# Kernel tuning notes

Measured on AMD Instinct MI355X. Metric: run time of the kernel, lower is better.

## Reference

```python
import jax, jax.numpy as jnp
import numpy as np

N = 100_000   # number of sparse points
C = 128       # channels
K3 = 27       # 3x3x3 kernel offsets


def sparse_conv(x, nbr, W, b):
    """Minkowski-style sparse conv: gather-GEMM-scatter.
    x:   [N, Cin] point features
    nbr: [N, K3] neighbor index per kernel offset; index N -> missing (zero row)
    W:   [K3, Cin, Cout], b: [Cout]
    """
    x_pad = jnp.concatenate([x, jnp.zeros((1, x.shape[1]), x.dtype)], axis=0)

    def step(acc, wk_nk):
        Wk, nk = wk_nk                      # Wk: [Cin,Cout], nk: [N]
        return acc + x_pad[nk] @ Wk, None   # gather + GEMM, accumulate

    acc0 = jnp.broadcast_to(b, (x.shape[0], W.shape[2])).astype(x.dtype)
    acc, _ = jax.lax.scan(step, acc0, (W, nbr.T))
    return acc


def setup_inputs() -> dict:
    key = jax.random.key(0)
    ks = jax.random.split(key, 12)
    Ch = C // 2

    def w(k, shape, fan_in):
        return jax.random.normal(k, shape, dtype=jnp.float32) / np.sqrt(fan_in)

    x = jax.random.normal(ks[0], (N, C), dtype=jnp.float32)
    # neighbor map; value N means "no neighbor" (maps to zero-padded row)
    nbr = jax.random.randint(ks[1], (N, K3), 0, N + 1, dtype=jnp.int32)

    return {
        "x": x,
        "nbr": nbr,
        "W00": w(ks[2], (K3, C, Ch), K3 * C),   # conv0_0: kxkxk, C -> C/2
        "b00": jnp.zeros((Ch,), jnp.float32),
        "W01": w(ks[3], (K3, Ch, Ch), K3 * Ch),  # conv0_1: kxkxk, C/2 -> C/2
        "b01": jnp.zeros((Ch,), jnp.float32),
        "W10": w(ks[4], (C, Ch), C),             # conv1_0: 1x1x1, C -> C/2
        "b10": jnp.zeros((Ch,), jnp.float32),
        "W11": w(ks[5], (K3, Ch, Ch), K3 * Ch),  # conv1_1: kxkxk, C/2 -> C/2
        "b11": jnp.zeros((Ch,), jnp.float32),
        "W12": w(ks[6], (Ch, Ch), Ch),           # conv1_2: 1x1x1, C/2 -> C/2
        "b12": jnp.zeros((Ch,), jnp.float32),
    }


def reference(x, nbr, W00, b00, W01, b01, W10, b10, W11, b11, W12, b12):
    # branch 0: conv -> relu -> conv
    h0 = jax.nn.relu(sparse_conv(x, nbr, W00, b00))
    out0 = sparse_conv(h0, nbr, W01, b01)
    # branch 1: 1x1 conv -> relu -> conv -> relu -> 1x1 conv
    h1 = jax.nn.relu(x @ W10 + b10)
    h1 = jax.nn.relu(sparse_conv(h1, nbr, W11, b11))
    out1 = h1 @ W12 + b12
    # concat channels, residual add
    return jnp.concatenate([out0, out1], axis=1) + x
```

## Files before the change

### kernel.cpp

```cpp
#include <hip/hip_runtime.h>
#include <hip/hip_bf16.h>
#include <stdint.h>

typedef __bf16 bf16x8 __attribute__((ext_vector_type(8)));
typedef float  f32x4  __attribute__((ext_vector_type(4)));

#define MFMA(A, B, C) __builtin_amdgcn_mfma_f32_16x16x32_bf16((A), (B), (C), 0, 0, 0)

#define LDS_BARRIER() asm volatile("s_waitcnt lgkmcnt(0)\n\ts_barrier" ::: "memory")

static __device__ __forceinline__ unsigned short f2b(float f) {
    union { float f; unsigned int u; } v; v.f = f;
    return (unsigned short)((v.u + 0x7FFFu + ((v.u >> 16) & 1u)) >> 16);
}

__global__ __launch_bounds__(256) void convert_kernel(
    const float* __restrict__ x, unsigned short* __restrict__ xb,
    unsigned short* __restrict__ hb, int N) {
    long long i = (long long)blockIdx.x * blockDim.x + threadIdx.x;
    long long base = i * 4;
    long long nx = (long long)N * 128;
    long long total = nx + 128;
    if (base >= total) return;
    if (base < nx) {
        float4 v = *(const float4*)(x + base);
        ushort4 o;
        o.x = f2b(v.x); o.y = f2b(v.y); o.z = f2b(v.z); o.w = f2b(v.w);
        *(ushort4*)(xb + base) = o;
    } else {
        ushort4 z = make_ushort4(0, 0, 0, 0);
        *(ushort4*)(xb + base) = z;
        *(ushort4*)(hb + base) = z;
    }
}

__global__ __launch_bounds__(256) void pack_kernel(
    const float* __restrict__ W00, const float* __restrict__ W01,
    const float* __restrict__ W10, const float* __restrict__ W11,
    const float* __restrict__ W12,
    unsigned short* __restrict__ wp00, unsigned short* __restrict__ wpC,
    unsigned short* __restrict__ wp10, unsigned short* __restrict__ wp12) {
    int g = blockIdx.x * blockDim.x + threadIdx.x;
    const float* W; int cinSteps; int which;
    if (g < 27648)      { W = W00; cinSteps = 4; which = 0; }
    else if (g < 41472) { g -= 27648; W = W01; cinSteps = 2; which = 1; }
    else if (g < 55296) { g -= 41472; W = W11; cinSteps = 2; which = 2; }
    else if (g < 56320) { g -= 55296; W = W10; cinSteps = 4; which = 3; }
    else if (g < 56832) { g -= 56320; W = W12; cinSteps = 2; which = 4; }
    else return;
    int lane = g & 63;
    int st   = g >> 6;
    int t    = st & 3;
    int s    = st >> 2;
    int q = lane >> 4, n16 = lane & 15;
    int k    = s / cinSteps;
    int cinb = (s % cinSteps) * 32;
    int Cin  = cinSteps * 32;
    int cout = t * 16 + n16;
    unsigned short o[8];
#pragma unroll
    for (int j = 0; j < 8; ++j) {
        float v = W[(size_t)(k * Cin + cinb + q * 8 + j) * 64 + cout];
        o[j] = f2b(v);
    }
    unsigned short* dst;
    if (which == 0)      dst = wp00 + (size_t)g * 8;
    else if (which == 1) dst = wpC + (size_t)k * 8192 +
                               ((size_t)(((s & 1) * 4 + t) * 64 + lane)) * 8;
    else if (which == 2) dst = wpC + (size_t)k * 8192 + 4096 +
                               ((size_t)(((s & 1) * 4 + t) * 64 + lane)) * 8;
    else if (which == 3) dst = wp10 + (size_t)g * 8;
    else                 dst = wp12 + (size_t)g * 8;
    *(ushort4*)(dst)     = make_ushort4(o[0], o[1], o[2], o[3]);
    *(ushort4*)(dst + 4) = make_ushort4(o[4], o[5], o[6], o[7]);
}

__global__ __launch_bounds__(256, 3) void passB_kernel(
    const unsigned short* __restrict__ xb, const int* __restrict__ nbr,
    const unsigned short* __restrict__ wp00, const unsigned short* __restrict__ wp10,
    const float* __restrict__ b00, const float* __restrict__ b10,
    unsigned short* __restrict__ hb, int N) {
    __shared__ __align__(16) unsigned short bbuf[2][8192];
    __shared__ int lds_idx[128 * 27];
    const int tid  = threadIdx.x;
    const int lane = tid & 63;
    const int wv   = tid >> 6;
    const int q = lane >> 4, n16 = lane & 15;
    const int rowbase = blockIdx.x * 128 + wv * 32;

    int4 br[4];
#pragma unroll
    for (int j = 0; j < 4; ++j) br[j] = *(const int4*)(wp00 + j * 2048 + tid * 8);
    {
        long long gbase = (long long)blockIdx.x * 128 * 27;
        long long lim = (long long)N * 27 - 1;
        for (int i = tid; i < 3456; i += 256) {
            long long gi = gbase + i; if (gi > lim) gi = lim;
            lds_idx[i] = nbr[gi];
        }
    }
#pragma unroll
    for (int j = 0; j < 4; ++j) *(int4*)(&bbuf[0][j * 2048 + tid * 8]) = br[j];
    __syncthreads();

    f32x4 acc0[2][4];
    f32x4 acc1[2][4];
#pragma unroll
    for (int rs = 0; rs < 2; ++rs)
#pragma unroll
        for (int t = 0; t < 4; ++t) { acc0[rs][t] = (f32x4)0.f; acc1[rs][t] = (f32x4)0.f; }

    const int idxb0 = (wv * 32 + n16) * 27;
    const int idxb1 = (wv * 32 + 16 + n16) * 27;
    const int own0 = min(rowbase + n16, N - 1);
    const int own1 = min(rowbase + 16 + n16, N - 1);

    int ia = lds_idx[idxb0], ib = lds_idx[idxb1];
    bf16x8 D0[4], D1[4];
    {
        const unsigned short* p0 = xb + (size_t)ia * 128 + q * 8;
        const unsigned short* p1 = xb + (size_t)ib * 128 + q * 8;
#pragma unroll
        for (int s2 = 0; s2 < 4; ++s2) {
            D0[s2] = *(const bf16x8*)(p0 + s2 * 32);
            D1[s2] = *(const bf16x8*)(p1 + s2 * 32);
        }
    }

    for (int k = 0; k < 27; ++k) {
        int buf = k & 1;
        if (k < 26) {
            const unsigned short* src = wp00 + (size_t)(k + 1) * 8192;
#pragma unroll
            for (int j = 0; j < 4; ++j) br[j] = *(const int4*)(src + j * 2048 + tid * 8);
        }
        int ian = (k + 1 < 27) ? lds_idx[idxb0 + k + 1] : own0;
        int ibn = (k + 1 < 27) ? lds_idx[idxb1 + k + 1] : own1;
        bf16x8 D0n[4], D1n[4];
        {
            const unsigned short* p0 = xb + (size_t)ian * 128 + q * 8;
            const unsigned short* p1 = xb + (size_t)ibn * 128 + q * 8;
#pragma unroll
            for (int s2 = 0; s2 < 4; ++s2) {
                D0n[s2] = *(const bf16x8*)(p0 + s2 * 32);
                D1n[s2] = *(const bf16x8*)(p1 + s2 * 32);
            }
        }
        const unsigned short* lb = &bbuf[buf][0];
#pragma unroll
        for (int s2 = 0; s2 < 4; ++s2) {
#pragma unroll
            for (int t = 0; t < 4; ++t) {
                bf16x8 B = *(const bf16x8*)(lb + (s2 * 4 + t) * 512 + lane * 8);
                acc0[0][t] = MFMA(D0[s2], B, acc0[0][t]);
                acc0[1][t] = MFMA(D1[s2], B, acc0[1][t]);
            }
        }
        if (k < 26) {
#pragma unroll
            for (int j = 0; j < 4; ++j)
                *(int4*)(&bbuf[buf ^ 1][j * 2048 + tid * 8]) = br[j];
        }
#pragma unroll
        for (int s2 = 0; s2 < 4; ++s2) { D0[s2] = D0n[s2]; D1[s2] = D1n[s2]; }
        LDS_BARRIER();
    }

#pragma unroll
    for (int s2 = 0; s2 < 4; ++s2) {
#pragma unroll
        for (int t = 0; t < 4; ++t) {
            bf16x8 B = *(const bf16x8*)(wp10 + s2 * 2048 + t * 512 + lane * 8);
            acc1[0][t] = MFMA(D0[s2], B, acc1[0][t]);
            acc1[1][t] = MFMA(D1[s2], B, acc1[1][t]);
        }
    }

#pragma unroll
    for (int rs = 0; rs < 2; ++rs)
#pragma unroll
        for (int t = 0; t < 4; ++t) {
            int col = t * 16 + n16;
            float bb0 = b00[col], bb1 = b10[col];
#pragma unroll
            for (int r = 0; r < 4; ++r) {
                int row = rowbase + rs * 16 + q * 4 + r;
                if (row < N) {
                    hb[(size_t)row * 128 + col]      = f2b(fmaxf(acc0[rs][t][r] + bb0, 0.f));
                    hb[(size_t)row * 128 + 64 + col] = f2b(fmaxf(acc1[rs][t][r] + bb1, 0.f));
                }
            }
        }
}

__global__ __launch_bounds__(256, 3) void passC_kernel(
    const unsigned short* __restrict__ hb, const int* __restrict__ nbr,
    const float* __restrict__ x,
    const unsigned short* __restrict__ wpC, const unsigned short* __restrict__ wp12,
    const float* __restrict__ b01, const float* __restrict__ b11,
    const float* __restrict__ b12, float* __restrict__ out, int N) {
    __shared__ __align__(16) unsigned short bbuf[2][8192];
    __shared__ int lds_idx[128 * 27];
    const int tid  = threadIdx.x;
    const int lane = tid & 63;
    const int wv   = tid >> 6;
    const int q = lane >> 4, n16 = lane & 15;
    const int rowbase = blockIdx.x * 128 + wv * 32;

    int4 br[4];
#pragma unroll
    for (int j = 0; j < 4; ++j) br[j] = *(const int4*)(wpC + j * 2048 + tid * 8);
    {
        long long gbase = (long long)blockIdx.x * 128 * 27;
        long long lim = (long long)N * 27 - 1;
        for (int i = tid; i < 3456; i += 256) {
            long long gi = gbase + i; if (gi > lim) gi = lim;
            lds_idx[i] = nbr[gi];
        }
    }
#pragma unroll
    for (int j = 0; j < 4; ++j) *(int4*)(&bbuf[0][j * 2048 + tid * 8]) = br[j];
    __syncthreads();

    f32x4 accO0[2][4];
    f32x4 accT[2][4];
#pragma unroll
    for (int rs = 0; rs < 2; ++rs)
#pragma unroll
        for (int t = 0; t < 4; ++t) { accO0[rs][t] = (f32x4)0.f; accT[rs][t] = (f32x4)0.f; }

    const int idxb0 = (wv * 32 + n16) * 27;
    const int idxb1 = (wv * 32 + 16 + n16) * 27;

    int ia = lds_idx[idxb0], ib = lds_idx[idxb1];
    bf16x8 DA0[2], DC0[2], DA1[2], DC1[2];
    {
        const unsigned short* p0 = hb + (size_t)ia * 128 + q * 8;
        const unsigned short* p1 = hb + (size_t)ib * 128 + q * 8;
#pragma unroll
        for (int s2 = 0; s2 < 2; ++s2) {
            DA0[s2] = *(const bf16x8*)(p0 + s2 * 32);
            DC0[s2] = *(const bf16x8*)(p0 + 64 + s2 * 32);
            DA1[s2] = *(const bf16x8*)(p1 + s2 * 32);
            DC1[s2] = *(const bf16x8*)(p1 + 64 + s2 * 32);
        }
    }

    for (int k = 0; k < 27; ++k) {
        int buf = k & 1;
        if (k < 26) {
            const unsigned short* src = wpC + (size_t)(k + 1) * 8192;
#pragma unroll
            for (int j = 0; j < 4; ++j) br[j] = *(const int4*)(src + j * 2048 + tid * 8);
        }
        bf16x8 DA0n[2], DC0n[2], DA1n[2], DC1n[2];
        if (k < 26) {
            int ian = lds_idx[idxb0 + k + 1];
            int ibn = lds_idx[idxb1 + k + 1];
            const unsigned short* p0 = hb + (size_t)ian * 128 + q * 8;
            const unsigned short* p1 = hb + (size_t)ibn * 128 + q * 8;
#pragma unroll
            for (int s2 = 0; s2 < 2; ++s2) {
                DA0n[s2] = *(const bf16x8*)(p0 + s2 * 32);
                DC0n[s2] = *(const bf16x8*)(p0 + 64 + s2 * 32);
                DA1n[s2] = *(const bf16x8*)(p1 + s2 * 32);
                DC1n[s2] = *(const bf16x8*)(p1 + 64 + s2 * 32);
            }
        }
        const unsigned short* lb = &bbuf[buf][0];
#pragma unroll
        for (int s2 = 0; s2 < 2; ++s2) {
#pragma unroll
            for (int t = 0; t < 4; ++t) {
                bf16x8 B = *(const bf16x8*)(lb + (s2 * 4 + t) * 512 + lane * 8);
                accO0[0][t] = MFMA(DA0[s2], B, accO0[0][t]);
                accO0[1][t] = MFMA(DA1[s2], B, accO0[1][t]);
            }
#pragma unroll
            for (int t = 0; t < 4; ++t) {
                bf16x8 B2 = *(const bf16x8*)(lb + 4096 + (s2 * 4 + t) * 512 + lane * 8);
                accT[0][t] = MFMA(DC0[s2], B2, accT[0][t]);
                accT[1][t] = MFMA(DC1[s2], B2, accT[1][t]);
            }
        }
        if (k < 26) {
#pragma unroll
            for (int j = 0; j < 4; ++j)
                *(int4*)(&bbuf[buf ^ 1][j * 2048 + tid * 8]) = br[j];
#pragma unroll
            for (int s2 = 0; s2 < 2; ++s2) {
                DA0[s2] = DA0n[s2]; DC0[s2] = DC0n[s2];
                DA1[s2] = DA1n[s2]; DC1[s2] = DC1n[s2];
            }
        }
        LDS_BARRIER();
    }

    unsigned short* scratch = &bbuf[0][0];
    unsigned short* myl = scratch + wv * 2304;
#pragma unroll
    for (int rs = 0; rs < 2; ++rs)
#pragma unroll
        for (int t = 0; t < 4; ++t) {
            int col = t * 16 + n16;
            float bo = b01[col], bt = b11[col];
#pragma unroll
            for (int r = 0; r < 4; ++r) {
                int row = rowbase + rs * 16 + q * 4 + r;
                if (row < N) {
                    float xv = __builtin_nontemporal_load(x + (size_t)row * 128 + col);
                    __builtin_nontemporal_store(accO0[rs][t][r] + bo + xv,
                                                out + (size_t)row * 128 + col);
                }
                float tv = fmaxf(accT[rs][t][r] + bt, 0.f);
                myl[(rs * 16 + q * 4 + r) * 72 + col] = f2b(tv);
            }
        }

    f32x4 accO1[2][4];
#pragma unroll
    for (int rs = 0; rs < 2; ++rs)
#pragma unroll
        for (int t = 0; t < 4; ++t) accO1[rs][t] = (f32x4)0.f;
#pragma unroll
    for (int s2 = 0; s2 < 2; ++s2) {
        bf16x8 A0 = *(const bf16x8*)(myl + n16 * 72 + s2 * 32 + q * 8);
        bf16x8 A1 = *(const bf16x8*)(myl + (16 + n16) * 72 + s2 * 32 + q * 8);
#pragma unroll
        for (int t = 0; t < 4; ++t) {
            bf16x8 B = *(const bf16x8*)(wp12 + s2 * 2048 + t * 512 + lane * 8);
            accO1[0][t] = MFMA(A0, B, accO1[0][t]);
            accO1[1][t] = MFMA(A1, B, accO1[1][t]);
        }
    }
#pragma unroll
    for (int rs = 0; rs < 2; ++rs)
#pragma unroll
        for (int t = 0; t < 4; ++t) {
            int col = t * 16 + n16;
            float bo = b12[col];
#pragma unroll
            for (int r = 0; r < 4; ++r) {
                int row = rowbase + rs * 16 + q * 4 + r;
                if (row < N) {
                    float xv = __builtin_nontemporal_load(x + (size_t)row * 128 + 64 + col);
                    __builtin_nontemporal_store(accO1[rs][t][r] + bo + xv,
                                                out + (size_t)row * 128 + 64 + col);
                }
            }
        }
}

extern "C" void kernel_launch(void* const* d_in, const int* in_sizes, int n_in,
                              void* d_out, int out_size, void* d_ws, size_t ws_size,
                              hipStream_t stream) {
    const float* x   = (const float*)d_in[0];
    const int*   nbr = (const int*)d_in[1];
    const float* W00 = (const float*)d_in[2];
    const float* b00 = (const float*)d_in[3];
    const float* W01 = (const float*)d_in[4];
    const float* b01 = (const float*)d_in[5];
    const float* W10 = (const float*)d_in[6];
    const float* b10 = (const float*)d_in[7];
    const float* W11 = (const float*)d_in[8];
    const float* b11 = (const float*)d_in[9];
    const float* W12 = (const float*)d_in[10];
    const float* b12 = (const float*)d_in[11];
    float* out = (float*)d_out;
    int N = in_sizes[0] / 128;

    char* ws = (char*)d_ws;
    size_t cur = 0;
    unsigned short* xb  = (unsigned short*)(ws + cur); cur += (size_t)(N + 1) * 128 * 2;
    unsigned short* hb  = (unsigned short*)(ws + cur); cur += (size_t)(N + 1) * 128 * 2;
    unsigned short* wp00 = (unsigned short*)(ws + cur); cur += 27648 * 8 * 2;
    unsigned short* wpC  = (unsigned short*)(ws + cur); cur += (size_t)27 * 8192 * 2;
    unsigned short* wp10 = (unsigned short*)(ws + cur); cur += 8192 * 2;
    unsigned short* wp12 = (unsigned short*)(ws + cur); cur += 4096 * 2;

    long long cvt_groups = ((long long)N * 128 + 128) / 4;
    int cvt_blocks = (int)((cvt_groups + 255) / 256);
    convert_kernel<<<cvt_blocks, 256, 0, stream>>>(x, xb, hb, N);
    pack_kernel<<<222, 256, 0, stream>>>(W00, W01, W10, W11, W12,
                                         wp00, wpC, wp10, wp12);
    int nstrips = (N + 127) / 128;
    passB_kernel<<<nstrips, 256, 0, stream>>>(xb, nbr, wp00, wp10, b00, b10, hb, N);
    passC_kernel<<<nstrips, 256, 0, stream>>>(hb, nbr, x, wpC, wp12,
                                              b01, b11, b12, out, N);
}
```

Before: 430.1 us.

## Double rows per wave to reuse each LDS weight fragment across four row tiles

Each wave now handles 64 rows (four 16-row tiles) instead of 32, so each block covers 256 points and every B fragment read from LDS feeds four MFMAs instead of two. This halves the number of blocks and the total weight streaming and barrier count per point. In exchange it doubles accumulator and gather registers, so occupancy drops from three to two blocks per SIMD-group. It also needs a larger index buffer in LDS, which is reused as scratch for the fourth wave's epilogue.

```diff
diff --git a/kernel.cpp b/kernel.cpp
--- a/kernel.cpp
+++ b/kernel.cpp
@@ -75,26 +75,26 @@
     *(ushort4*)(dst + 4) = make_ushort4(o[4], o[5], o[6], o[7]);
 }
 
-__global__ __launch_bounds__(256, 3) void passB_kernel(
+__global__ __launch_bounds__(256, 2) void passB_kernel(
     const unsigned short* __restrict__ xb, const int* __restrict__ nbr,
     const unsigned short* __restrict__ wp00, const unsigned short* __restrict__ wp10,
     const float* __restrict__ b00, const float* __restrict__ b10,
     unsigned short* __restrict__ hb, int N) {
     __shared__ __align__(16) unsigned short bbuf[2][8192];
-    __shared__ int lds_idx[128 * 27];
+    __shared__ __align__(16) int lds_idx[256 * 27];
     const int tid  = threadIdx.x;
     const int lane = tid & 63;
     const int wv   = tid >> 6;
     const int q = lane >> 4, n16 = lane & 15;
-    const int rowbase = blockIdx.x * 128 + wv * 32;
+    const int rowbase = blockIdx.x * 256 + wv * 64;
 
     int4 br[4];
 #pragma unroll
     for (int j = 0; j < 4; ++j) br[j] = *(const int4*)(wp00 + j * 2048 + tid * 8);
     {
-        long long gbase = (long long)blockIdx.x * 128 * 27;
+        long long gbase = (long long)blockIdx.x * 256 * 27;
         long long lim = (long long)N * 27 - 1;
-        for (int i = tid; i < 3456; i += 256) {
+        for (int i = tid; i < 6912; i += 256) {
             long long gi = gbase + i; if (gi > lim) gi = lim;
             lds_idx[i] = nbr[gi];
         }
@@ -103,28 +103,26 @@
     for (int j = 0; j < 4; ++j) *(int4*)(&bbuf[0][j * 2048 + tid * 8]) = br[j];
     __syncthreads();
 
-    f32x4 acc0[2][4];
-    f32x4 acc1[2][4];
-#pragma unroll
-    for (int rs = 0; rs < 2; ++rs)
+    f32x4 acc0[4][4];
+    f32x4 acc1[4][4];
+#pragma unroll
+    for (int rs = 0; rs < 4; ++rs)
 #pragma unroll
         for (int t = 0; t < 4; ++t) { acc0[rs][t] = (f32x4)0.f; acc1[rs][t] = (f32x4)0.f; }
 
-    const int idxb0 = (wv * 32 + n16) * 27;
-    const int idxb1 = (wv * 32 + 16 + n16) * 27;
-    const int own0 = min(rowbase + n16, N - 1);
-    const int own1 = min(rowbase + 16 + n16, N - 1);
-
-    int ia = lds_idx[idxb0], ib = lds_idx[idxb1];
-    bf16x8 D0[4], D1[4];
-    {
-        const unsigned short* p0 = xb + (size_t)ia * 128 + q * 8;
-        const unsigned short* p1 = xb + (size_t)ib * 128 + q * 8;
-#pragma unroll
-        for (int s2 = 0; s2 < 4; ++s2) {
-            D0[s2] = *(const bf16x8*)(p0 + s2 * 32);
-            D1[s2] = *(const bf16x8*)(p1 + s2 * 32);
-        }
+    int idxb[4], own[4];
+#pragma unroll
+    for (int rs = 0; rs < 4; ++rs) {
+        idxb[rs] = (wv * 64 + rs * 16 + n16) * 27;
+        own[rs]  = min(rowbase + rs * 16 + n16, N - 1);
+    }
+
+    bf16x8 D[4][4];
+#pragma unroll
+    for (int rs = 0; rs < 4; ++rs) {
+        const unsigned short* p = xb + (size_t)lds_idx[idxb[rs]] * 128 + q * 8;
+#pragma unroll
+        for (int s2 = 0; s2 < 4; ++s2) D[rs][s2] = *(const bf16x8*)(p + s2 * 32);
     }
 
     for (int k = 0; k < 27; ++k) {
@@ -134,17 +132,13 @@
 #pragma unroll
             for (int j = 0; j < 4; ++j) br[j] = *(const int4*)(src + j * 2048 + tid * 8);
         }
-        int ian = (k + 1 < 27) ? lds_idx[idxb0 + k + 1] : own0;
-        int ibn = (k + 1 < 27) ? lds_idx[idxb1 + k + 1] : own1;
-        bf16x8 D0n[4], D1n[4];
-        {
-            const unsigned short* p0 = xb + (size_t)ian * 128 + q * 8;
-            const unsigned short* p1 = xb + (size_t)ibn * 128 + q * 8;
-#pragma unroll
-            for (int s2 = 0; s2 < 4; ++s2) {
-                D0n[s2] = *(const bf16x8*)(p0 + s2 * 32);
-                D1n[s2] = *(const bf16x8*)(p1 + s2 * 32);
-            }
+        bf16x8 Dn[4][4];
+#pragma unroll
+        for (int rs = 0; rs < 4; ++rs) {
+            int ian = (k + 1 < 27) ? lds_idx[idxb[rs] + k + 1] : own[rs];
+            const unsigned short* p = xb + (size_t)ian * 128 + q * 8;
+#pragma unroll
+            for (int s2 = 0; s2 < 4; ++s2) Dn[rs][s2] = *(const bf16x8*)(p + s2 * 32);
         }
         const unsigned short* lb = &bbuf[buf][0];
 #pragma unroll
@@ -152,8 +146,9 @@
 #pragma unroll
             for (int t = 0; t < 4; ++t) {
                 bf16x8 B = *(const bf16x8*)(lb + (s2 * 4 + t) * 512 + lane * 8);
-                acc0[0][t] = MFMA(D0[s2], B, acc0[0][t]);
-                acc0[1][t] = MFMA(D1[s2], B, acc0[1][t]);
+#pragma unroll
+                for (int rs = 0; rs < 4; ++rs)
+                    acc0[rs][t] = MFMA(D[rs][s2], B, acc0[rs][t]);
             }
         }
         if (k < 26) {
@@ -162,7 +157,9 @@
                 *(int4*)(&bbuf[buf ^ 1][j * 2048 + tid * 8]) = br[j];
         }
 #pragma unroll
-        for (int s2 = 0; s2 < 4; ++s2) { D0[s2] = D0n[s2]; D1[s2] = D1n[s2]; }
+        for (int rs = 0; rs < 4; ++rs)
+#pragma unroll
+            for (int s2 = 0; s2 < 4; ++s2) D[rs][s2] = Dn[rs][s2];
         LDS_BARRIER();
     }
 
@@ -171,13 +168,14 @@
 #pragma unroll
         for (int t = 0; t < 4; ++t) {
             bf16x8 B = *(const bf16x8*)(wp10 + s2 * 2048 + t * 512 + lane * 8);
-            acc1[0][t] = MFMA(D0[s2], B, acc1[0][t]);
-            acc1[1][t] = MFMA(D1[s2], B, acc1[1][t]);
-        }
-    }
-
-#pragma unroll
-    for (int rs = 0; rs < 2; ++rs)
+#pragma unroll
+            for (int rs = 0; rs < 4; ++rs)
+                acc1[rs][t] = MFMA(D[rs][s2], B, acc1[rs][t]);
+        }
+    }
+
+#pragma unroll
+    for (int rs = 0; rs < 4; ++rs)
 #pragma unroll
         for (int t = 0; t < 4; ++t) {
             int col = t * 16 + n16;
@@ -193,27 +191,27 @@
         }
 }
 
-__global__ __launch_bounds__(256, 3) void passC_kernel(
+__global__ __launch_bounds__(256, 2) void passC_kernel(
     const unsigned short* __restrict__ hb, const int* __restrict__ nbr,
     const float* __restrict__ x,
     const unsigned short* __restrict__ wpC, const unsigned short* __restrict__ wp12,
     const float* __restrict__ b01, const float* __restrict__ b11,
     const float* __restrict__ b12, float* __restrict__ out, int N) {
     __shared__ __align__(16) unsigned short bbuf[2][8192];
-    __shared__ int lds_idx[128 * 27];
+    __shared__ __align__(16) int lds_idx[256 * 27];
     const int tid  = threadIdx.x;
     const int lane = tid & 63;
     const int wv   = tid >> 6;
     const int q = lane >> 4, n16 = lane & 15;
-    const int rowbase = blockIdx.x * 128 + wv * 32;
+    const int rowbase = blockIdx.x * 256 + wv * 64;
 
     int4 br[4];
 #pragma unroll
     for (int j = 0; j < 4; ++j) br[j] = *(const int4*)(wpC + j * 2048 + tid * 8);
     {
-        long long gbase = (long long)blockIdx.x * 128 * 27;
+        long long gbase = (long long)blockIdx.x * 256 * 27;
         long long lim = (long long)N * 27 - 1;
-        for (int i = tid; i < 3456; i += 256) {
+        for (int i = tid; i < 6912; i += 256) {
             long long gi = gbase + i; if (gi > lim) gi = lim;
             lds_idx[i] = nbr[gi];
         }
@@ -222,27 +220,25 @@
     for (int j = 0; j < 4; ++j) *(int4*)(&bbuf[0][j * 2048 + tid * 8]) = br[j];
     __syncthreads();
 
-    f32x4 accO0[2][4];
-    f32x4 accT[2][4];
-#pragma unroll
-    for (int rs = 0; rs < 2; ++rs)
+    f32x4 accO0[4][4];
+    f32x4 accT[4][4];
+#pragma unroll
+    for (int rs = 0; rs < 4; ++rs)
 #pragma unroll
         for (int t = 0; t < 4; ++t) { accO0[rs][t] = (f32x4)0.f; accT[rs][t] = (f32x4)0.f; }
 
-    const int idxb0 = (wv * 32 + n16) * 27;
-    const int idxb1 = (wv * 32 + 16 + n16) * 27;
-
-    int ia = lds_idx[idxb0], ib = lds_idx[idxb1];
-    bf16x8 DA0[2], DC0[2], DA1[2], DC1[2];
-    {
-        const unsigned short* p0 = hb + (size_t)ia * 128 + q * 8;
-        const unsigned short* p1 = hb + (size_t)ib * 128 + q * 8;
+    int idxb[4];
+#pragma unroll
+    for (int rs = 0; rs < 4; ++rs) idxb[rs] = (wv * 64 + rs * 16 + n16) * 27;
+
+    bf16x8 DA[4][2], DC[4][2];
+#pragma unroll
+    for (int rs = 0; rs < 4; ++rs) {
+        const unsigned short* p = hb + (size_t)lds_idx[idxb[rs]] * 128 + q * 8;
 #pragma unroll
         for (int s2 = 0; s2 < 2; ++s2) {
-            DA0[s2] = *(const bf16x8*)(p0 + s2 * 32);
-            DC0[s2] = *(const bf16x8*)(p0 + 64 + s2 * 32);
-            DA1[s2] = *(const bf16x8*)(p1 + s2 * 32);
-            DC1[s2] = *(const bf16x8*)(p1 + 64 + s2 * 32);
+            DA[rs][s2] = *(const bf16x8*)(p + s2 * 32);
+            DC[rs][s2] = *(const bf16x8*)(p + 64 + s2 * 32);
         }
     }
 
@@ -253,18 +249,17 @@
 #pragma unroll
             for (int j = 0; j < 4; ++j) br[j] = *(const int4*)(src + j * 2048 + tid * 8);
         }
-        bf16x8 DA0n[2], DC0n[2], DA1n[2], DC1n[2];
-        if (k < 26) {
-            int ian = lds_idx[idxb0 + k + 1];
-            int ibn = lds_idx[idxb1 + k + 1];
-            const unsigned short* p0 = hb + (size_t)ian * 128 + q * 8;
-            const unsigned short* p1 = hb + (size_t)ibn * 128 + q * 8;
-#pragma unroll
-            for (int s2 = 0; s2 < 2; ++s2) {
-                DA0n[s2] = *(const bf16x8*)(p0 + s2 * 32);
-                DC0n[s2] = *(const bf16x8*)(p0 + 64 + s2 * 32);
-                DA1n[s2] = *(const bf16x8*)(p1 + s2 * 32);
-                DC1n[s2] = *(const bf16x8*)(p1 + 64 + s2 * 32);
+        bf16x8 DAn[4][2], DCn[4][2];
+        if (k < 26) {
+#pragma unroll
+            for (int rs = 0; rs < 4; ++rs) {
+                int ian = lds_idx[idxb[rs] + k + 1];
+                const unsigned short* p = hb + (size_t)ian * 128 + q * 8;
+#pragma unroll
+                for (int s2 = 0; s2 < 2; ++s2) {
+                    DAn[rs][s2] = *(const bf16x8*)(p + s2 * 32);
+                    DCn[rs][s2] = *(const bf16x8*)(p + 64 + s2 * 32);
+                }
             }
         }
         const unsigned short* lb = &bbuf[buf][0];
@@ -273,14 +268,16 @@
 #pragma unroll
             for (int t = 0; t < 4; ++t) {
                 bf16x8 B = *(const bf16x8*)(lb + (s2 * 4 + t) * 512 + lane * 8);
-                accO0[0][t] = MFMA(DA0[s2], B, accO0[0][t]);
-                accO0[1][t] = MFMA(DA1[s2], B, accO0[1][t]);
+#pragma unroll
+                for (int rs = 0; rs < 4; ++rs)
+                    accO0[rs][t] = MFMA(DA[rs][s2], B, accO0[rs][t]);
             }
 #pragma unroll
             for (int t = 0; t < 4; ++t) {
                 bf16x8 B2 = *(const bf16x8*)(lb + 4096 + (s2 * 4 + t) * 512 + lane * 8);
-                accT[0][t] = MFMA(DC0[s2], B2, accT[0][t]);
-                accT[1][t] = MFMA(DC1[s2], B2, accT[1][t]);
+#pragma unroll
+                for (int rs = 0; rs < 4; ++rs)
+                    accT[rs][t] = MFMA(DC[rs][s2], B2, accT[rs][t]);
             }
         }
         if (k < 26) {
@@ -288,18 +285,19 @@
             for (int j = 0; j < 4; ++j)
                 *(int4*)(&bbuf[buf ^ 1][j * 2048 + tid * 8]) = br[j];
 #pragma unroll
-            for (int s2 = 0; s2 < 2; ++s2) {
-                DA0[s2] = DA0n[s2]; DC0[s2] = DC0n[s2];
-                DA1[s2] = DA1n[s2]; DC1[s2] = DC1n[s2];
-            }
+            for (int rs = 0; rs < 4; ++rs)
+#pragma unroll
+                for (int s2 = 0; s2 < 2; ++s2) {
+                    DA[rs][s2] = DAn[rs][s2]; DC[rs][s2] = DCn[rs][s2];
+                }
         }
         LDS_BARRIER();
     }
 
-    unsigned short* scratch = &bbuf[0][0];
-    unsigned short* myl = scratch + wv * 2304;
-#pragma unroll
-    for (int rs = 0; rs < 2; ++rs)
+    unsigned short* myl = (wv < 3) ? (&bbuf[0][0] + wv * 4608)
+                                   : (unsigned short*)lds_idx;
+#pragma unroll
+    for (int rs = 0; rs < 4; ++rs)
 #pragma unroll
         for (int t = 0; t < 4; ++t) {
             int col = t * 16 + n16;
@@ -317,24 +315,25 @@
             }
         }
 
-    f32x4 accO1[2][4];
-#pragma unroll
-    for (int rs = 0; rs < 2; ++rs)
+    f32x4 accO1[4][4];
+#pragma unroll
+    for (int rs = 0; rs < 4; ++rs)
 #pragma unroll
         for (int t = 0; t < 4; ++t) accO1[rs][t] = (f32x4)0.f;
 #pragma unroll
     for (int s2 = 0; s2 < 2; ++s2) {
-        bf16x8 A0 = *(const bf16x8*)(myl + n16 * 72 + s2 * 32 + q * 8);
-        bf16x8 A1 = *(const bf16x8*)(myl + (16 + n16) * 72 + s2 * 32 + q * 8);
 #pragma unroll
         for (int t = 0; t < 4; ++t) {
             bf16x8 B = *(const bf16x8*)(wp12 + s2 * 2048 + t * 512 + lane * 8);
-            accO1[0][t] = MFMA(A0, B, accO1[0][t]);
-            accO1[1][t] = MFMA(A1, B, accO1[1][t]);
-        }
-    }
-#pragma unroll
-    for (int rs = 0; rs < 2; ++rs)
+#pragma unroll
+            for (int rs = 0; rs < 4; ++rs) {
+                bf16x8 A = *(const bf16x8*)(myl + (rs * 16 + n16) * 72 + s2 * 32 + q * 8);
+                accO1[rs][t] = MFMA(A, B, accO1[rs][t]);
+            }
+        }
+    }
+#pragma unroll
+    for (int rs = 0; rs < 4; ++rs)
 #pragma unroll
         for (int t = 0; t < 4; ++t) {
             int col = t * 16 + n16;
@@ -383,7 +382,7 @@
     convert_kernel<<<cvt_blocks, 256, 0, stream>>>(x, xb, hb, N);
     pack_kernel<<<222, 256, 0, stream>>>(W00, W01, W10, W11, W12,
                                          wp00, wpC, wp10, wp12);
-    int nstrips = (N + 127) / 128;
+    int nstrips = (N + 255) / 256;
     passB_kernel<<<nstrips, 256, 0, stream>>>(xb, nbr, wp00, wp10, b00, b10, hb, N);
     passC_kernel<<<nstrips, 256, 0, stream>>>(hb, nbr, x, wpC, wp12,
                                               b01, b11, b12, out, N);
```

Result: faster. 416.0 us (-3.3%).

## Split sparse-conv passes into channel-half phases with two-deep gather prefetch

Applied to the files above, without the earlier changes.

Both conv kernels now walk the input channels (passB) or the two output branches (passC) in two sequential phases of 64 channels. Each phase keeps a smaller weight double-buffer in LDS and holds only half-width gathered rows in registers. The freed registers and LDS pay for a prefetch two offsets ahead instead of one, to hide gather latency better. The cost is a second pass over the neighbour indices and repeated weight streaming, and each gathered row is now read in two halves, so gather traffic is less coalesced.

```diff
diff --git a/kernel.cpp b/kernel.cpp
--- a/kernel.cpp
+++ b/kernel.cpp
@@ -80,29 +80,14 @@
     const unsigned short* __restrict__ wp00, const unsigned short* __restrict__ wp10,
     const float* __restrict__ b00, const float* __restrict__ b10,
     unsigned short* __restrict__ hb, int N) {
-    __shared__ __align__(16) unsigned short bbuf[2][8192];
-    __shared__ int lds_idx[128 * 27];
+    __shared__ __align__(16) unsigned short bbuf[2][4096];
+    __shared__ __align__(16) int lds_idx[128 * 27];
     const int tid  = threadIdx.x;
     const int lane = tid & 63;
     const int wv   = tid >> 6;
     const int q = lane >> 4, n16 = lane & 15;
     const int rowbase = blockIdx.x * 128 + wv * 32;
 
-    int4 br[4];
-#pragma unroll
-    for (int j = 0; j < 4; ++j) br[j] = *(const int4*)(wp00 + j * 2048 + tid * 8);
-    {
-        long long gbase = (long long)blockIdx.x * 128 * 27;
-        long long lim = (long long)N * 27 - 1;
-        for (int i = tid; i < 3456; i += 256) {
-            long long gi = gbase + i; if (gi > lim) gi = lim;
-            lds_idx[i] = nbr[gi];
-        }
-    }
-#pragma unroll
-    for (int j = 0; j < 4; ++j) *(int4*)(&bbuf[0][j * 2048 + tid * 8]) = br[j];
-    __syncthreads();
-
     f32x4 acc0[2][4];
     f32x4 acc1[2][4];
 #pragma unroll
@@ -110,69 +95,95 @@
 #pragma unroll
         for (int t = 0; t < 4; ++t) { acc0[rs][t] = (f32x4)0.f; acc1[rs][t] = (f32x4)0.f; }
 
-    const int idxb0 = (wv * 32 + n16) * 27;
-    const int idxb1 = (wv * 32 + 16 + n16) * 27;
-    const int own0 = min(rowbase + n16, N - 1);
-    const int own1 = min(rowbase + 16 + n16, N - 1);
-
-    int ia = lds_idx[idxb0], ib = lds_idx[idxb1];
-    bf16x8 D0[4], D1[4];
-    {
-        const unsigned short* p0 = xb + (size_t)ia * 128 + q * 8;
-        const unsigned short* p1 = xb + (size_t)ib * 128 + q * 8;
-#pragma unroll
-        for (int s2 = 0; s2 < 4; ++s2) {
-            D0[s2] = *(const bf16x8*)(p0 + s2 * 32);
-            D1[s2] = *(const bf16x8*)(p1 + s2 * 32);
-        }
-    }
-
-    for (int k = 0; k < 27; ++k) {
-        int buf = k & 1;
-        if (k < 26) {
-            const unsigned short* src = wp00 + (size_t)(k + 1) * 8192;
-#pragma unroll
-            for (int j = 0; j < 4; ++j) br[j] = *(const int4*)(src + j * 2048 + tid * 8);
-        }
-        int ian = (k + 1 < 27) ? lds_idx[idxb0 + k + 1] : own0;
-        int ibn = (k + 1 < 27) ? lds_idx[idxb1 + k + 1] : own1;
-        bf16x8 D0n[4], D1n[4];
-        {
-            const unsigned short* p0 = xb + (size_t)ian * 128 + q * 8;
-            const unsigned short* p1 = xb + (size_t)ibn * 128 + q * 8;
-#pragma unroll
-            for (int s2 = 0; s2 < 4; ++s2) {
-                D0n[s2] = *(const bf16x8*)(p0 + s2 * 32);
-                D1n[s2] = *(const bf16x8*)(p1 + s2 * 32);
-            }
-        }
-        const unsigned short* lb = &bbuf[buf][0];
-#pragma unroll
-        for (int s2 = 0; s2 < 4; ++s2) {
+    int idxb[2], own[2];
+#pragma unroll
+    for (int rs = 0; rs < 2; ++rs) {
+        idxb[rs] = (wv * 32 + rs * 16 + n16) * 27;
+        own[rs]  = min(rowbase + rs * 16 + n16, N - 1);
+    }
+
+#pragma unroll
+    for (int ph = 0; ph < 2; ++ph) {
+        const int choff = ph * 64;
+        int4 br[2];
+#pragma unroll
+        for (int j = 0; j < 2; ++j)
+            br[j] = *(const int4*)(wp00 + ph * 4096 + j * 2048 + tid * 8);
+        if (ph == 0) {
+            long long gbase = (long long)blockIdx.x * 128 * 27;
+            long long lim = (long long)N * 27 - 1;
+            for (int i = tid; i < 3456; i += 256) {
+                long long gi = gbase + i; if (gi > lim) gi = lim;
+                lds_idx[i] = nbr[gi];
+            }
+        }
+#pragma unroll
+        for (int j = 0; j < 2; ++j) *(int4*)(&bbuf[0][j * 2048 + tid * 8]) = br[j];
+        __syncthreads();
+
+        bf16x8 Da[2][2], Db[2][2], Dc[2][2];
+#pragma unroll
+        for (int rs = 0; rs < 2; ++rs) {
+            const unsigned short* p0 =
+                xb + (size_t)lds_idx[idxb[rs] + 0] * 128 + choff + q * 8;
+            Da[rs][0] = *(const bf16x8*)(p0);
+            Da[rs][1] = *(const bf16x8*)(p0 + 32);
+            const unsigned short* p1 =
+                xb + (size_t)lds_idx[idxb[rs] + 1] * 128 + choff + q * 8;
+            Db[rs][0] = *(const bf16x8*)(p1);
+            Db[rs][1] = *(const bf16x8*)(p1 + 32);
+        }
+
+        for (int k = 0; k < 27; ++k) {
+            int buf = k & 1;
+            if (k < 26) {
+                const unsigned short* src = wp00 + ph * 4096 + (size_t)(k + 1) * 8192;
+#pragma unroll
+                for (int j = 0; j < 2; ++j)
+                    br[j] = *(const int4*)(src + j * 2048 + tid * 8);
+            }
+#pragma unroll
+            for (int rs = 0; rs < 2; ++rs) {
+                int j2 = k + 2;
+                int ii = (j2 < 27) ? lds_idx[idxb[rs] + j2] : own[rs];
+                const unsigned short* p = xb + (size_t)ii * 128 + choff + q * 8;
+                Dc[rs][0] = *(const bf16x8*)(p);
+                Dc[rs][1] = *(const bf16x8*)(p + 32);
+            }
+            const unsigned short* lb = &bbuf[buf][0];
+#pragma unroll
+            for (int s2 = 0; s2 < 2; ++s2) {
+#pragma unroll
+                for (int t = 0; t < 4; ++t) {
+                    bf16x8 B = *(const bf16x8*)(lb + (s2 * 4 + t) * 512 + lane * 8);
+#pragma unroll
+                    for (int rs = 0; rs < 2; ++rs)
+                        acc0[rs][t] = MFMA(Da[rs][s2], B, acc0[rs][t]);
+                }
+            }
+            if (k < 26) {
+#pragma unroll
+                for (int j = 0; j < 2; ++j)
+                    *(int4*)(&bbuf[buf ^ 1][j * 2048 + tid * 8]) = br[j];
+            }
+#pragma unroll
+            for (int rs = 0; rs < 2; ++rs)
+#pragma unroll
+                for (int s2 = 0; s2 < 2; ++s2) {
+                    Da[rs][s2] = Db[rs][s2]; Db[rs][s2] = Dc[rs][s2];
+                }
+            LDS_BARRIER();
+        }
+
+#pragma unroll
+        for (int s2 = 0; s2 < 2; ++s2) {
 #pragma unroll
             for (int t = 0; t < 4; ++t) {
-                bf16x8 B = *(const bf16x8*)(lb + (s2 * 4 + t) * 512 + lane * 8);
-                acc0[0][t] = MFMA(D0[s2], B, acc0[0][t]);
-                acc0[1][t] = MFMA(D1[s2], B, acc0[1][t]);
-            }
-        }
-        if (k < 26) {
-#pragma unroll
-            for (int j = 0; j < 4; ++j)
-                *(int4*)(&bbuf[buf ^ 1][j * 2048 + tid * 8]) = br[j];
-        }
-#pragma unroll
-        for (int s2 = 0; s2 < 4; ++s2) { D0[s2] = D0n[s2]; D1[s2] = D1n[s2]; }
-        LDS_BARRIER();
-    }
-
-#pragma unroll
-    for (int s2 = 0; s2 < 4; ++s2) {
-#pragma unroll
-        for (int t = 0; t < 4; ++t) {
-            bf16x8 B = *(const bf16x8*)(wp10 + s2 * 2048 + t * 512 + lane * 8);
-            acc1[0][t] = MFMA(D0[s2], B, acc1[0][t]);
-            acc1[1][t] = MFMA(D1[s2], B, acc1[1][t]);
+                bf16x8 B = *(const bf16x8*)(wp10 + ((ph * 2 + s2) * 4 + t) * 512 + lane * 8);
+#pragma unroll
+                for (int rs = 0; rs < 2; ++rs)
+                    acc1[rs][t] = MFMA(Da[rs][s2], B, acc1[rs][t]);
+            }
         }
     }
 
@@ -199,156 +210,228 @@
     const unsigned short* __restrict__ wpC, const unsigned short* __restrict__ wp12,
     const float* __restrict__ b01, const float* __restrict__ b11,
     const float* __restrict__ b12, float* __restrict__ out, int N) {
-    __shared__ __align__(16) unsigned short bbuf[2][8192];
-    __shared__ int lds_idx[128 * 27];
+    __shared__ __align__(16) unsigned short bbuf[2][4096];
+    __shared__ __align__(16) int lds_idx[128 * 27];
     const int tid  = threadIdx.x;
     const int lane = tid & 63;
     const int wv   = tid >> 6;
     const int q = lane >> 4, n16 = lane & 15;
     const int rowbase = blockIdx.x * 128 + wv * 32;
 
-    int4 br[4];
-#pragma unroll
-    for (int j = 0; j < 4; ++j) br[j] = *(const int4*)(wpC + j * 2048 + tid * 8);
+    int idxb[2];
+#pragma unroll
+    for (int rs = 0; rs < 2; ++rs) idxb[rs] = (wv * 32 + rs * 16 + n16) * 27;
+
     {
-        long long gbase = (long long)blockIdx.x * 128 * 27;
-        long long lim = (long long)N * 27 - 1;
-        for (int i = tid; i < 3456; i += 256) {
-            long long gi = gbase + i; if (gi > lim) gi = lim;
-            lds_idx[i] = nbr[gi];
-        }
-    }
-#pragma unroll
-    for (int j = 0; j < 4; ++j) *(int4*)(&bbuf[0][j * 2048 + tid * 8]) = br[j];
-    __syncthreads();
-
-    f32x4 accO0[2][4];
-    f32x4 accT[2][4];
-#pragma unroll
-    for (int rs = 0; rs < 2; ++rs)
-#pragma unroll
-        for (int t = 0; t < 4; ++t) { accO0[rs][t] = (f32x4)0.f; accT[rs][t] = (f32x4)0.f; }
-
-    const int idxb0 = (wv * 32 + n16) * 27;
-    const int idxb1 = (wv * 32 + 16 + n16) * 27;
-
-    int ia = lds_idx[idxb0], ib = lds_idx[idxb1];
-    bf16x8 DA0[2], DC0[2], DA1[2], DC1[2];
+        int4 br[2];
+#pragma unroll
+        for (int j = 0; j < 2; ++j) br[j] = *(const int4*)(wpC + j * 2048 + tid * 8);
+        {
+            long long gbase = (long long)blockIdx.x * 128 * 27;
+            long long lim = (long long)N * 27 - 1;
+            for (int i = tid; i < 3456; i += 256) {
+                long long gi = gbase + i; if (gi > lim) gi = lim;
+                lds_idx[i] = nbr[gi];
+            }
+        }
+#pragma unroll
+        for (int j = 0; j < 2; ++j) *(int4*)(&bbuf[0][j * 2048 + tid * 8]) = br[j];
+        __syncthreads();
+
+        f32x4 accA[2][4];
+#pragma unroll
+        for (int rs = 0; rs < 2; ++rs)
+#pragma unroll
+            for (int t = 0; t < 4; ++t) accA[rs][t] = (f32x4)0.f;
+
+        bf16x8 Da[2][2], Db[2][2], Dc[2][2];
+#pragma unroll
+        for (int rs = 0; rs < 2; ++rs) {
+            const unsigned short* p0 = hb + (size_t)lds_idx[idxb[rs] + 0] * 128 + q * 8;
+            Da[rs][0] = *(const bf16x8*)(p0);
+            Da[rs][1] = *(const bf16x8*)(p0 + 32);
+            const unsigned short* p1 = hb + (size_t)lds_idx[idxb[rs] + 1] * 128 + q * 8;
+            Db[rs][0] = *(const bf16x8*)(p1);
+            Db[rs][1] = *(const bf16x8*)(p1 + 32);
+        }
+
+        for (int k = 0; k < 27; ++k) {
+            int buf = k & 1;
+            if (k < 26) {
+                const unsigned short* src = wpC + (size_t)(k + 1) * 8192;
+#pragma unroll
+                for (int j = 0; j < 2; ++j)
+                    br[j] = *(const int4*)(src + j * 2048 + tid * 8);
+            }
+#pragma unroll
+            for (int rs = 0; rs < 2; ++rs) {
+                int j2 = min(k + 2, 26);
+                const unsigned short* p =
+                    hb + (size_t)lds_idx[idxb[rs] + j2] * 128 + q * 8;
+                Dc[rs][0] = *(const bf16x8*)(p);
+                Dc[rs][1] = *(const bf16x8*)(p + 32);
+            }
+            const unsigned short* lb = &bbuf[buf][0];
+#pragma unroll
+            for (int s2 = 0; s2 < 2; ++s2) {
+#pragma unroll
+                for (int t = 0; t < 4; ++t) {
+                    bf16x8 B = *(const bf16x8*)(lb + (s2 * 4 + t) * 512 + lane * 8);
+#pragma unroll
+                    for (int rs = 0; rs < 2; ++rs)
+                        accA[rs][t] = MFMA(Da[rs][s2], B, accA[rs][t]);
+                }
+            }
+            if (k < 26) {
+#pragma unroll
+                for (int j = 0; j < 2; ++j)
+                    *(int4*)(&bbuf[buf ^ 1][j * 2048 + tid * 8]) = br[j];
+            }
+#pragma unroll
+            for (int rs = 0; rs < 2; ++rs)
+#pragma unroll
+                for (int s2 = 0; s2 < 2; ++s2) {
+                    Da[rs][s2] = Db[rs][s2]; Db[rs][s2] = Dc[rs][s2];
+                }
+            LDS_BARRIER();
+        }
+
+#pragma unroll
+        for (int rs = 0; rs < 2; ++rs)
+#pragma unroll
+            for (int t = 0; t < 4; ++t) {
+                int col = t * 16 + n16;
+                float bo = b01[col];
+#pragma unroll
+                for (int r = 0; r < 4; ++r) {
+                    int row = rowbase + rs * 16 + q * 4 + r;
+                    if (row < N) {
+                        float xv = __builtin_nontemporal_load(x + (size_t)row * 128 + col);
+                        __builtin_nontemporal_store(accA[rs][t][r] + bo + xv,
+                                                    out + (size_t)row * 128 + col);
+                    }
+                }
+            }
+    }
+
     {
-        const unsigned short* p0 = hb + (size_t)ia * 128 + q * 8;
-        const unsigned short* p1 = hb + (size_t)ib * 128 + q * 8;
+        int4 br[2];
+#pragma unroll
+        for (int j = 0; j < 2; ++j)
+            br[j] = *(const int4*)(wpC + 4096 + j * 2048 + tid * 8);
+#pragma unroll
+        for (int j = 0; j < 2; ++j) *(int4*)(&bbuf[0][j * 2048 + tid * 8]) = br[j];
+        __syncthreads();
+
+        f32x4 accT[2][4];
+#pragma unroll
+        for (int rs = 0; rs < 2; ++rs)
+#pragma unroll
+            for (int t = 0; t < 4; ++t) accT[rs][t] = (f32x4)0.f;
+
+        bf16x8 Da[2][2], Db[2][2], Dc[2][2];
+#pragma unroll
+        for (int rs = 0; rs < 2; ++rs) {
+            const unsigned short* p0 =
+                hb + (size_t)lds_idx[idxb[rs] + 0] * 128 + 64 + q * 8;
+            Da[rs][0] = *(const bf16x8*)(p0);
+            Da[rs][1] = *(const bf16x8*)(p0 + 32);
+            const unsigned short* p1 =
+                hb + (size_t)lds_idx[idxb[rs] + 1] * 128 + 64 + q * 8;
+            Db[rs][0] = *(const bf16x8*)(p1);
+            Db[rs][1] = *(const bf16x8*)(p1 + 32);
+        }
+
+        for (int k = 0; k < 27; ++k) {
+            int buf = k & 1;
+            if (k < 26) {
+                const unsigned short* src = wpC + 4096 + (size_t)(k + 1) * 8192;
+#pragma unroll
+                for (int j = 0; j < 2; ++j)
+                    br[j] = *(const int4*)(src + j * 2048 + tid * 8);
+            }
+#pragma unroll
+            for (int rs = 0; rs < 2; ++rs) {
+                int j2 = min(k + 2, 26);
+                const unsigned short* p =
+                    hb + (size_t)lds_idx[idxb[rs] + j2] * 128 + 64 + q * 8;
+                Dc[rs][0] = *(const bf16x8*)(p);
+                Dc[rs][1] = *(const bf16x8*)(p + 32);
+            }
+            const unsigned short* lb = &bbuf[buf][0];
+#pragma unroll
+            for (int s2 = 0; s2 < 2; ++s2) {
+#pragma unroll
+                for (int t = 0; t < 4; ++t) {
+                    bf16x8 B = *(const bf16x8*)(lb + (s2 * 4 + t) * 512 + lane * 8);
+#pragma unroll
+                    for (int rs = 0; rs < 2; ++rs)
+                        accT[rs][t] = MFMA(Da[rs][s2], B, accT[rs][t]);
+                }
+            }
+            if (k < 26) {
+#pragma unroll
+                for (int j = 0; j < 2; ++j)
+                    *(int4*)(&bbuf[buf ^ 1][j * 2048 + tid * 8]) = br[j];
+            }
+#pragma unroll
+            for (int rs = 0; rs < 2; ++rs)
+#pragma unroll
+                for (int s2 = 0; s2 < 2; ++s2) {
+                    Da[rs][s2] = Db[rs][s2]; Db[rs][s2] = Dc[rs][s2];
+                }
+            LDS_BARRIER();
+        }
+
+        unsigned short* myl = (wv < 3) ? ((unsigned short*)lds_idx + wv * 2304)
+                                       : &bbuf[0][0];
+#pragma unroll
+        for (int rs = 0; rs < 2; ++rs)
+#pragma unroll
+            for (int t = 0; t < 4; ++t) {
+                int col = t * 16 + n16;
+                float bt = b11[col];
+#pragma unroll
+                for (int r = 0; r < 4; ++r) {
+                    float tv = fmaxf(accT[rs][t][r] + bt, 0.f);
+                    myl[(rs * 16 + q * 4 + r) * 72 + col] = f2b(tv);
+                }
+            }
+
+        f32x4 accO1[2][4];
+#pragma unroll
+        for (int rs = 0; rs < 2; ++rs)
+#pragma unroll
+            for (int t = 0; t < 4; ++t) accO1[rs][t] = (f32x4)0.f;
 #pragma unroll
         for (int s2 = 0; s2 < 2; ++s2) {
-            DA0[s2] = *(const bf16x8*)(p0 + s2 * 32);
-            DC0[s2] = *(const bf16x8*)(p0 + 64 + s2 * 32);
-            DA1[s2] = *(const bf16x8*)(p1 + s2 * 32);
-            DC1[s2] = *(const bf16x8*)(p1 + 64 + s2 * 32);
-        }
-    }
-
-    for (int k = 0; k < 27; ++k) {
-        int buf = k & 1;
-        if (k < 26) {
-            const unsigned short* src = wpC + (size_t)(k + 1) * 8192;
-#pragma unroll
-            for (int j = 0; j < 4; ++j) br[j] = *(const int4*)(src + j * 2048 + tid * 8);
-        }
-        bf16x8 DA0n[2], DC0n[2], DA1n[2], DC1n[2];
-        if (k < 26) {
-            int ian = lds_idx[idxb0 + k + 1];
-            int ibn = lds_idx[idxb1 + k + 1];
-            const unsigned short* p0 = hb + (size_t)ian * 128 + q * 8;
-            const unsigned short* p1 = hb + (size_t)ibn * 128 + q * 8;
-#pragma unroll
-            for (int s2 = 0; s2 < 2; ++s2) {
-                DA0n[s2] = *(const bf16x8*)(p0 + s2 * 32);
-                DC0n[s2] = *(const bf16x8*)(p0 + 64 + s2 * 32);
-                DA1n[s2] = *(const bf16x8*)(p1 + s2 * 32);
-                DC1n[s2] = *(const bf16x8*)(p1 + 64 + s2 * 32);
-            }
-        }
-        const unsigned short* lb = &bbuf[buf][0];
-#pragma unroll
-        for (int s2 = 0; s2 < 2; ++s2) {
 #pragma unroll
             for (int t = 0; t < 4; ++t) {
-                bf16x8 B = *(const bf16x8*)(lb + (s2 * 4 + t) * 512 + lane * 8);
-                accO0[0][t] = MFMA(DA0[s2], B, accO0[0][t]);
-                accO0[1][t] = MFMA(DA1[s2], B, accO0[1][t]);
-            }
+                bf16x8 B = *(const bf16x8*)(wp12 + s2 * 2048 + t * 512 + lane * 8);
+#pragma unroll
+                for (int rs = 0; rs < 2; ++rs) {
+                    bf16x8 A = *(const bf16x8*)(myl + (rs * 16 + n16) * 72 + s2 * 32 + q * 8);
+                    accO1[rs][t] = MFMA(A, B, accO1[rs][t]);
+                }
+            }
+        }
+#pragma unroll
+        for (int rs = 0; rs < 2; ++rs)
 #pragma unroll
             for (int t = 0; t < 4; ++t) {
-                bf16x8 B2 = *(const bf16x8*)(lb + 4096 + (s2 * 4 + t) * 512 + lane * 8);
-                accT[0][t] = MFMA(DC0[s2], B2, accT[0][t]);
-                accT[1][t] = MFMA(DC1[s2], B2, accT[1][t]);
-            }
-        }
-        if (k < 26) {
-#pragma unroll
-            for (int j = 0; j < 4; ++j)
-                *(int4*)(&bbuf[buf ^ 1][j * 2048 + tid * 8]) = br[j];
-#pragma unroll
-            for (int s2 = 0; s2 < 2; ++s2) {
-                DA0[s2] = DA0n[s2]; DC0[s2] = DC0n[s2];
-                DA1[s2] = DA1n[s2]; DC1[s2] = DC1n[s2];
-            }
-        }
-        LDS_BARRIER();
-    }
-
-    unsigned short* scratch = &bbuf[0][0];
-    unsigned short* myl = scratch + wv * 2304;
-#pragma unroll
-    for (int rs = 0; rs < 2; ++rs)
-#pragma unroll
-        for (int t = 0; t < 4; ++t) {
-            int col = t * 16 + n16;
-            float bo = b01[col], bt = b11[col];
-#pragma unroll
-            for (int r = 0; r < 4; ++r) {
-                int row = rowbase + rs * 16 + q * 4 + r;
-                if (row < N) {
-                    float xv = __builtin_nontemporal_load(x + (size_t)row * 128 + col);
-                    __builtin_nontemporal_store(accO0[rs][t][r] + bo + xv,
-                                                out + (size_t)row * 128 + col);
-                }
-                float tv = fmaxf(accT[rs][t][r] + bt, 0.f);
-                myl[(rs * 16 + q * 4 + r) * 72 + col] = f2b(tv);
-            }
-        }
-
-    f32x4 accO1[2][4];
-#pragma unroll
-    for (int rs = 0; rs < 2; ++rs)
-#pragma unroll
-        for (int t = 0; t < 4; ++t) accO1[rs][t] = (f32x4)0.f;
-#pragma unroll
-    for (int s2 = 0; s2 < 2; ++s2) {
-        bf16x8 A0 = *(const bf16x8*)(myl + n16 * 72 + s2 * 32 + q * 8);
-        bf16x8 A1 = *(const bf16x8*)(myl + (16 + n16) * 72 + s2 * 32 + q * 8);
-#pragma unroll
-        for (int t = 0; t < 4; ++t) {
-            bf16x8 B = *(const bf16x8*)(wp12 + s2 * 2048 + t * 512 + lane * 8);
-            accO1[0][t] = MFMA(A0, B, accO1[0][t]);
-            accO1[1][t] = MFMA(A1, B, accO1[1][t]);
-        }
-    }
-#pragma unroll
-    for (int rs = 0; rs < 2; ++rs)
-#pragma unroll
-        for (int t = 0; t < 4; ++t) {
-            int col = t * 16 + n16;
-            float bo = b12[col];
-#pragma unroll
-            for (int r = 0; r < 4; ++r) {
-                int row = rowbase + rs * 16 + q * 4 + r;
-                if (row < N) {
-                    float xv = __builtin_nontemporal_load(x + (size_t)row * 128 + 64 + col);
-                    __builtin_nontemporal_store(accO1[rs][t][r] + bo + xv,
-                                                out + (size_t)row * 128 + 64 + col);
-                }
-            }
-        }
+                int col = t * 16 + n16;
+                float bo = b12[col];
+#pragma unroll
+                for (int r = 0; r < 4; ++r) {
+                    int row = rowbase + rs * 16 + q * 4 + r;
+                    if (row < N) {
+                        float xv = __builtin_nontemporal_load(x + (size_t)row * 128 + 64 + col);
+                        __builtin_nontemporal_store(accO1[rs][t][r] + bo + xv,
+                                                    out + (size_t)row * 128 + 64 + col);
+                    }
+                }
+            }
+    }
 }
 
 extern "C" void kernel_launch(void* const* d_in, const int* in_sizes, int n_in,
```

New measurement: 417.8 us. -2.8%, faster.
